# Performance work log

Hardware: AMD Instinct MI355X
Metric: run time of the kernel (lower is better)

Reference implementation:

```python
import jax, jax.numpy as jnp
import numpy as np

B, M, FIN, FOUT, K, E = 4, 50000, 128, 128, 4, 800000


def setup_inputs() -> dict:
    key = jax.random.key(0)
    ks = jax.random.split(key, 8)
    x = jax.random.normal(ks[0], (B, M, FIN), dtype=jnp.float32)
    L_rows = jax.random.randint(ks[1], (E,), 0, M, dtype=jnp.int32)
    L_cols = jax.random.randint(ks[2], (E,), 0, M, dtype=jnp.int32)
    # stands in for the rescaled (0.75 * (2L/lmax - I)) Laplacian values
    L_vals = jax.random.normal(ks[3], (E,), dtype=jnp.float32) * 0.05
    stddev = 1.0 / np.sqrt(FIN * (K + 0.5) / 2.0)
    kernel = jax.random.normal(ks[4], (K * FIN, FOUT), dtype=jnp.float32) * stddev
    W_down = jax.random.normal(ks[5], (FOUT, FOUT // 8), dtype=jnp.float32) * (1.0 / np.sqrt(FOUT))
    b_down = jnp.zeros((FOUT // 8,), dtype=jnp.float32)
    W_up = jax.random.normal(ks[6], (FOUT // 8, FOUT), dtype=jnp.float32) * (1.0 / np.sqrt(FOUT // 8))
    b_up = jnp.zeros((FOUT,), dtype=jnp.float32)
    return {"x": x, "L_vals": L_vals, "L_rows": L_rows, "L_cols": L_cols,
            "kernel": kernel, "W_down": W_down, "b_down": b_down,
            "W_up": W_up, "b_up": b_up}


def reference(x, L_vals, L_rows, L_cols, kernel, W_down, b_down, W_up, b_up):
    B_, M_, Fin = x.shape
    K_ = kernel.shape[0] // Fin

    def spmm(X):  # sparse L [M,M] @ dense X [M, D]
        return jax.ops.segment_sum(L_vals[:, None] * X[L_cols], L_rows, num_segments=M_)

    # Chebyshev recurrence, operating on [M, Fin*B] like the TF code
    x0 = x.transpose(1, 2, 0).reshape(M_, Fin * B_)
    stack = [x0]
    if K_ > 1:
        x1 = spmm(x0)
        stack.append(x1)
    for _ in range(2, K_):
        x2 = 2.0 * spmm(x1) - x0
        stack.append(x2)
        x0, x1 = x1, x2

    # [K,M,Fin*B] -> [K,M,Fin,B] -> [B,M,Fin,K] -> [B*M, Fin*K]
    xs = jnp.stack(stack, axis=0).reshape(K_, M_, Fin, B_)
    xs = xs.transpose(3, 1, 2, 0).reshape(B_ * M_, Fin * K_)
    y = (xs @ kernel).reshape(B_, M_, -1)
    y = jax.nn.relu(y)

    # SE block: avg-pool over nodes, down (swish), up (sigmoid), scale
    s = jnp.mean(y, axis=1, keepdims=True)          # [B, 1, Fout]
    d = jax.nn.swish(s @ W_down + b_down)           # [B, 1, Fout/8]
    u = jax.nn.sigmoid(d @ W_up + b_up)             # [B, 1, Fout]
    return y * u
```

## Files before the change

kernel.cpp:

```cpp
#include <hip/hip_runtime.h>
#include <hip/hip_bf16.h>

#define BB 4
#define MM 50000
#define FINF 128
#define FOUTF 128
#define KCH 4
#define EE 800000
#define NROWS (BB*MM)
#define XC 512
#define CD 512
#define SLABS 4
#define SC (XC/SLABS)
#define SCB 512
#define NSB ((MM + SCB - 1)/SCB)
#define GXB ((MM + 255)/256)

__device__ __forceinline__ float bf2f(unsigned short u){
    union{unsigned int i; float f;} v; v.i = ((unsigned int)u) << 16; return v.f;
}
__device__ __forceinline__ unsigned short f2bf(float f){
    union{float f; unsigned int i;} v; v.f = f;
    unsigned int r = v.i + 0x7FFF + ((v.i >> 16) & 1);
    return (unsigned short)(r >> 16);
}

typedef __bf16 bf16x8 __attribute__((ext_vector_type(8)));
typedef float  f32x4  __attribute__((ext_vector_type(4)));

__global__ __launch_bounds__(256) void k_init_x0(const float* __restrict__ x,
                                                 unsigned short* __restrict__ X0){
    int tid = blockIdx.x*256 + threadIdx.x;
    if (tid >= BB*MM*FINF/4) return;
    int f4 = tid & 31;
    int t  = tid >> 5;
    int m  = t % MM, b = t / MM;
    float4 v = ((const float4*)x)[tid];
    ushort4 o;
    o.x = f2bf(v.x); o.y = f2bf(v.y); o.z = f2bf(v.z); o.w = f2bf(v.w);
    *(ushort4*)(X0 + (size_t)m*XC + b*FINF + f4*4) = o;
}

__global__ __launch_bounds__(256) void k_prepw(const float* __restrict__ kern,
                                               unsigned short* __restrict__ Wt){
    int tid = blockIdx.x*256 + threadIdx.x;
    int c = tid & 511, n = tid >> 9;
    int kc = c >> 7, f = c & 127;
    int ns = n >> 4, l16 = n & 15;
    int ks = c >> 5, rem = c & 31, g = rem >> 3, j = rem & 7;
    int lane = g*16 + l16;
    Wt[((ns*16 + ks)*64 + lane)*8 + j] = f2bf(kern[(f*KCH + kc)*FOUTF + n]);
}

__global__ __launch_bounds__(256) void k_hist(const int* __restrict__ rows, int* __restrict__ counts){
    int e = blockIdx.x*256 + threadIdx.x;
    if (e < EE) atomicAdd(&counts[rows[e]], 1);
}

__global__ __launch_bounds__(256) void k_scanA(const int* __restrict__ counts, int* __restrict__ part){
    __shared__ int red[256];
    int b = blockIdx.x, t = threadIdx.x;
    int i = b*SCB + t;
    int s = 0;
    if (i < MM) s += counts[i];
    if (i + 256 < (b+1)*SCB && i + 256 < MM) s += counts[i+256];
    red[t] = s; __syncthreads();
    for (int d = 128; d > 0; d >>= 1){
        if (t < d) red[t] += red[t+d];
        __syncthreads();
    }
    if (t == 0) part[b] = red[0];
}

__global__ __launch_bounds__(128) void k_scanB(int* __restrict__ part){
    __shared__ int sh[128];
    int t = threadIdx.x;
    sh[t] = (t < NSB) ? part[t] : 0;
    __syncthreads();
    for (int d = 1; d < 128; d <<= 1){
        int v = (t >= d) ? sh[t-d] : 0;
        __syncthreads();
        sh[t] += v;
        __syncthreads();
    }
    if (t < NSB) part[t] = sh[t];
}

__global__ __launch_bounds__(256) void k_scanC(const int* __restrict__ counts, const int* __restrict__ part,
                                               int* __restrict__ offs, int* __restrict__ cursor){
    __shared__ int sh[256];
    int b = blockIdx.x, t = threadIdx.x;
    int base = (b == 0) ? 0 : part[b-1];
    int i0 = b*SCB + 2*t;
    int c0 = (i0     < MM) ? counts[i0]   : 0;
    int c1 = (i0 + 1 < MM) ? counts[i0+1] : 0;
    sh[t] = c0 + c1; __syncthreads();
    for (int d = 1; d < 256; d <<= 1){
        int v = (t >= d) ? sh[t-d] : 0;
        __syncthreads();
        sh[t] += v;
        __syncthreads();
    }
    int excl = base + sh[t] - (c0 + c1);
    if (i0 < MM){ offs[i0] = excl;      cursor[i0] = excl; }
    if (i0 + 1 < MM){ offs[i0+1] = excl + c0; cursor[i0+1] = excl + c0; }
    if (b == gridDim.x-1 && t == 255) offs[MM] = EE;
}

__global__ __launch_bounds__(256) void k_scatter(const int* __restrict__ rows, const int* __restrict__ cols,
                                                 const float* __restrict__ vals, int* __restrict__ cursor,
                                                 int2* __restrict__ edges){
    int e = blockIdx.x*256 + threadIdx.x;
    if (e >= EE) return;
    int r = rows[e];
    int pos = atomicAdd(&cursor[r], 1);
    edges[pos] = make_int2(cols[e], __float_as_int(vals[e]));
}

__global__ __launch_bounds__(256) void k_spmm_slab(const unsigned short* __restrict__ Xin,
                                                   const unsigned short* __restrict__ Xprev,
                                                   unsigned short* __restrict__ Xout,
                                                   const int* __restrict__ offs,
                                                   const int2* __restrict__ edges,
                                                   float alpha, int sub, int cbase){
    int m    = blockIdx.x*4 + (threadIdx.x >> 6);
    int lane = threadIdx.x & 63;
    size_t c0 = (size_t)cbase + lane*2;
    int start = offs[m], end = offs[m+1];
    float a0 = 0.f, a1 = 0.f;

    int nb = (end - start) & ~3;
    int burst_end = start + nb;
    int j = start;

    int2 ee[4];
    if (j < burst_end){
        #pragma unroll
        for (int q = 0; q < 4; ++q) ee[q] = edges[j+q];
    }
    while (j < burst_end){
        int2 e_[4];
        #pragma unroll
        for (int q = 0; q < 4; ++q) e_[q] = ee[q];
        j += 4;
        if (j < burst_end){
            #pragma unroll
            for (int q = 0; q < 4; ++q) ee[q] = edges[j+q];
        }
        ushort2 xv[4];
        #pragma unroll
        for (int q = 0; q < 4; ++q)
            xv[q] = *(const ushort2*)(Xin + (size_t)e_[q].x*XC + c0);
        #pragma unroll
        for (int q = 0; q < 4; ++q){
            float val = __int_as_float(e_[q].y);
            a0 += val*bf2f(xv[q].x); a1 += val*bf2f(xv[q].y);
        }
    }
    for (; j < end; ++j){
        int2 e = edges[j];
        float val = __int_as_float(e.y);
        ushort2 xv = *(const ushort2*)(Xin + (size_t)e.x*XC + c0);
        a0 += val*bf2f(xv.x); a1 += val*bf2f(xv.y);
    }

    a0 *= alpha; a1 *= alpha;
    if (sub){
        ushort2 pv = *(const ushort2*)(Xprev + (size_t)m*XC + c0);
        a0 -= bf2f(pv.x); a1 -= bf2f(pv.y);
    }
    ushort2 o; o.x = f2bf(a0); o.y = f2bf(a1);
    *(ushort2*)(Xout + (size_t)m*XC + c0) = o;
}

__global__ __launch_bounds__(256, 2) void k_gemm(const unsigned short* __restrict__ X0,
                                                 const unsigned short* __restrict__ X1,
                                                 const unsigned short* __restrict__ X2,
                                                 const unsigned short* __restrict__ X3,
                                                 const unsigned short* __restrict__ Wt,
                                                 float* __restrict__ Y,
                                                 float* __restrict__ Ypart){
    const int wave = threadIdx.x >> 6;
    const int lane = threadIdx.x & 63;
    const int l16  = lane & 15;
    const int g    = lane >> 4;
    const int bidx = blockIdx.y;
    const int m0   = blockIdx.x*256 + wave*64;

    int aoff[4];
    #pragma unroll
    for (int i = 0; i < 4; ++i){
        int mr = m0 + i*16 + l16;
        if (mr >= MM) mr = MM-1;
        aoff[i] = mr*XC + bidx*FINF + g*8;
    }

    const unsigned short* const Xs[4] = {X0, X1, X2, X3};

    f32x4 acc[4][8];
    #pragma unroll
    for (int i = 0; i < 4; ++i)
        #pragma unroll
        for (int j = 0; j < 8; ++j) acc[i][j] = (f32x4){0.f,0.f,0.f,0.f};

    bf16x8 a_cur[4], b_cur[8], a_nxt[4], b_nxt[8];

    {
        const unsigned short* Xb = Xs[0];
        #pragma unroll
        for (int i = 0; i < 4; ++i) a_cur[i] = *(const bf16x8*)(Xb + aoff[i]);
        #pragma unroll
        for (int ns = 0; ns < 8; ++ns) b_cur[ns] = *(const bf16x8*)(Wt + (ns*16)*512 + lane*8);
    }

    #pragma unroll
    for (int ks = 0; ks < 16; ++ks){
        if (ks < 15){
            const int kn = ks + 1;
            const unsigned short* Xb = Xs[kn >> 2];
            const int f0 = (kn & 3)*32;
            #pragma unroll
            for (int i = 0; i < 4; ++i) a_nxt[i] = *(const bf16x8*)(Xb + aoff[i] + f0);
            #pragma unroll
            for (int ns = 0; ns < 8; ++ns) b_nxt[ns] = *(const bf16x8*)(Wt + (ns*16 + kn)*512 + lane*8);
        }
        #pragma unroll
        for (int ns = 0; ns < 8; ++ns)
            #pragma unroll
            for (int i = 0; i < 4; ++i)
                acc[i][ns] = __builtin_amdgcn_mfma_f32_16x16x32_bf16(a_cur[i], b_cur[ns], acc[i][ns], 0, 0, 0);
        #pragma unroll
        for (int i = 0; i < 4; ++i) a_cur[i] = a_nxt[i];
        #pragma unroll
        for (int ns = 0; ns < 8; ++ns) b_cur[ns] = b_nxt[ns];
    }

    __shared__ float ldsum[4][FOUTF];
    float csum[8];
    #pragma unroll
    for (int ns = 0; ns < 8; ++ns) csum[ns] = 0.f;

    #pragma unroll
    for (int i = 0; i < 4; ++i){
        #pragma unroll
        for (int reg = 0; reg < 4; ++reg){
            int mr = m0 + i*16 + g*4 + reg;
            if (mr < MM){
                #pragma unroll
                for (int ns = 0; ns < 8; ++ns){
                    float v = acc[i][ns][reg];
                    v = v > 0.f ? v : 0.f;
                    Y[((size_t)bidx*MM + mr)*FOUTF + ns*16 + l16] = v;
                    csum[ns] += v;
                }
            }
        }
    }
    #pragma unroll
    for (int ns = 0; ns < 8; ++ns){
        float v = csum[ns];
        v += __shfl_xor(v, 16);
        v += __shfl_xor(v, 32);
        csum[ns] = v;
    }
    if (lane < 16){
        #pragma unroll
        for (int ns = 0; ns < 8; ++ns) ldsum[wave][ns*16 + lane] = csum[ns];
    }
    __syncthreads();
    int t = threadIdx.x;
    if (t < FOUTF){
        float s = ldsum[0][t] + ldsum[1][t] + ldsum[2][t] + ldsum[3][t];
        Ypart[((size_t)bidx*GXB + blockIdx.x)*FOUTF + t] = s;
    }
}

__global__ __launch_bounds__(128) void k_se(const float* __restrict__ Ypart,
                                            const float* __restrict__ Wd, const float* __restrict__ bd,
                                            const float* __restrict__ Wu, const float* __restrict__ bu,
                                            float* __restrict__ u){
    int b = blockIdx.x, t = threadIdx.x;
    __shared__ float sm[128];
    __shared__ float dsh[16];
    float s = 0.f;
    for (int j = 0; j < GXB; ++j) s += Ypart[((size_t)b*GXB + j)*FOUTF + t];
    sm[t] = s * (1.0f/MM);
    __syncthreads();
    if (t < 16){
        float a = bd[t];
        for (int f = 0; f < 128; ++f) a += sm[f]*Wd[f*16 + t];
        dsh[t] = a / (1.f + expf(-a));
    }
    __syncthreads();
    float a = bu[t];
    for (int j = 0; j < 16; ++j) a += dsh[j]*Wu[j*FOUTF + t];
    u[b*FOUTF + t] = 1.f/(1.f + expf(-a));
}

__global__ __launch_bounds__(256) void k_scale(const float* __restrict__ Y, const float* __restrict__ u,
                                               float* __restrict__ out){
    int tid = blockIdx.x*256 + threadIdx.x;
    if (tid >= NROWS*FOUTF/4) return;
    int b  = tid / (MM*FOUTF/4);
    int f4 = tid & 31;
    float4 yv = ((const float4*)Y)[tid];
    float4 uv = *(const float4*)(u + b*FOUTF + f4*4);
    float4 o;
    o.x = yv.x*uv.x; o.y = yv.y*uv.y; o.z = yv.z*uv.z; o.w = yv.w*uv.w;
    ((float4*)out)[tid] = o;
}

extern "C" void kernel_launch(void* const* d_in, const int* in_sizes, int n_in,
                              void* d_out, int out_size, void* d_ws, size_t ws_size,
                              hipStream_t stream){
    (void)in_sizes; (void)n_in; (void)out_size; (void)ws_size;
    const float* x    = (const float*)d_in[0];
    const float* lv   = (const float*)d_in[1];
    const int*   lr   = (const int*)d_in[2];
    const int*   lc   = (const int*)d_in[3];
    const float* kern = (const float*)d_in[4];
    const float* Wd   = (const float*)d_in[5];
    const float* bd   = (const float*)d_in[6];
    const float* Wu   = (const float*)d_in[7];
    const float* bu   = (const float*)d_in[8];
    float* out = (float*)d_out;

    char* w = (char*)d_ws;
    size_t off = 0;
    auto take = [&](size_t bytes)->char*{
        char* p = w + off; off += (bytes + 255) & ~(size_t)255; return p;
    };
    unsigned short* X[4];
    for (int i = 0; i < 4; ++i) X[i] = (unsigned short*)take((size_t)MM*XC*2);
    float* Y           = (float*)take((size_t)NROWS*FOUTF*4);
    unsigned short* Wt = (unsigned short*)take((size_t)FOUTF*CD*2);
    int* counts        = (int*)take((size_t)MM*4);
    int* offs          = (int*)take((size_t)(MM+1)*4);
    int* cursor        = (int*)take((size_t)MM*4);
    int2* edges        = (int2*)take((size_t)EE*8);
    int* part          = (int*)take((size_t)NSB*4);
    float* Ypart       = (float*)take((size_t)BB*GXB*FOUTF*4);
    float* u           = (float*)take((size_t)BB*FOUTF*4);

    hipMemsetAsync(counts, 0, MM*4, stream);

    k_init_x0<<<25000, 256, 0, stream>>>(x, X[0]);
    k_prepw<<<256, 256, 0, stream>>>(kern, Wt);
    k_hist<<<(EE+255)/256, 256, 0, stream>>>(lr, counts);
    k_scanA<<<NSB, 256, 0, stream>>>(counts, part);
    k_scanB<<<1, 128, 0, stream>>>(part);
    k_scanC<<<NSB, 256, 0, stream>>>(counts, part, offs, cursor);
    k_scatter<<<(EE+255)/256, 256, 0, stream>>>(lr, lc, lv, cursor, edges);

    for (int s = 0; s < SLABS; ++s){
        int cbase = s*SC;
        k_spmm_slab<<<MM/4, 256, 0, stream>>>(X[0], X[0], X[1], offs, edges, 1.0f, 0, cbase);
        k_spmm_slab<<<MM/4, 256, 0, stream>>>(X[1], X[0], X[2], offs, edges, 2.0f, 1, cbase);
        k_spmm_slab<<<MM/4, 256, 0, stream>>>(X[2], X[1], X[3], offs, edges, 2.0f, 1, cbase);
    }

    dim3 ggemm(GXB, BB);
    k_gemm<<<ggemm, 256, 0, stream>>>(X[0], X[1], X[2], X[3], Wt, Y, Ypart);

    k_se<<<BB, 128, 0, stream>>>(Ypart, Wd, bd, Wu, bu, u);
    k_scale<<<25000, 256, 0, stream>>>(Y, u, out);
}
```

Before: 833.0 us.

## Stage GEMM A/B tiles through swizzled double-buffered LDS via direct global-to-LDS loads

The dense Chebyshev GEMM now copies the A (node features) and B (weights) tiles into two LDS buffers with `global_load_lds`, instead of each wave loading its operands straight into registers. The A tile uses an XOR swizzle so the later LDS reads avoid bank conflicts. Each weight tile is now loaded once per block and shared across all four waves, where before every wave fetched it separately. The cost is two barriers per k-step, more LDS use that may reduce occupancy, and reliance on the barrier to wait for the async LDS writes.

```diff
diff --git a/kernel.cpp b/kernel.cpp
--- a/kernel.cpp
+++ b/kernel.cpp
@@ -28,6 +28,9 @@
 typedef __bf16 bf16x8 __attribute__((ext_vector_type(8)));
 typedef float  f32x4  __attribute__((ext_vector_type(4)));
 
+typedef __attribute__((address_space(3))) unsigned int       lds_uint;
+typedef const __attribute__((address_space(1))) unsigned int gbl_uint;
+
 __global__ __launch_bounds__(256) void k_init_x0(const float* __restrict__ x,
                                                  unsigned short* __restrict__ X0){
     int tid = blockIdx.x*256 + threadIdx.x;
@@ -185,15 +188,10 @@
     const int l16  = lane & 15;
     const int g    = lane >> 4;
     const int bidx = blockIdx.y;
-    const int m0   = blockIdx.x*256 + wave*64;
-
-    int aoff[4];
-    #pragma unroll
-    for (int i = 0; i < 4; ++i){
-        int mr = m0 + i*16 + l16;
-        if (mr >= MM) mr = MM-1;
-        aoff[i] = mr*XC + bidx*FINF + g*8;
-    }
+    const int m0   = blockIdx.x*256;
+
+    __shared__ unsigned short As[2][8192];
+    __shared__ unsigned short Bs[2][4096];
 
     const unsigned short* const Xs[4] = {X0, X1, X2, X3};
 
@@ -203,36 +201,49 @@
         #pragma unroll
         for (int j = 0; j < 8; ++j) acc[i][j] = (f32x4){0.f,0.f,0.f,0.f};
 
-    bf16x8 a_cur[4], b_cur[8], a_nxt[4], b_nxt[8];
-
-    {
-        const unsigned short* Xb = Xs[0];
-        #pragma unroll
-        for (int i = 0; i < 4; ++i) a_cur[i] = *(const bf16x8*)(Xb + aoff[i]);
-        #pragma unroll
-        for (int ns = 0; ns < 8; ++ns) b_cur[ns] = *(const bf16x8*)(Wt + (ns*16)*512 + lane*8);
-    }
-
-    #pragma unroll
+    auto stage = [&](int buf, int ks){
+        const unsigned short* Xb = Xs[ks >> 2];
+        const int f0 = (ks & 3)*64;
+        #pragma unroll
+        for (int q = 0; q < 4; ++q){
+            int row = q*64 + wave*16 + (lane >> 2);
+            int mr  = m0 + row; if (mr >= MM) mr = MM-1;
+            int inner = ((lane & 3)*16) ^ ((row & 6) << 3);
+            const char* src = (const char*)Xb + (size_t)mr*1024 + bidx*256 + f0 + inner;
+            lds_uint* dst = (lds_uint*)(&As[buf][(q*4096 + wave*1024)/2]);
+            __builtin_amdgcn_global_load_lds((gbl_uint*)src, dst, 16, 0, 0);
+        }
+        #pragma unroll
+        for (int q = 0; q < 2; ++q){
+            int ns = q*4 + wave;
+            const char* src = (const char*)Wt + (size_t)(ns*16 + ks)*1024 + lane*16;
+            lds_uint* dst = (lds_uint*)(&Bs[buf][ns*512]);
+            __builtin_amdgcn_global_load_lds((gbl_uint*)src, dst, 16, 0, 0);
+        }
+    };
+
+    stage(0, 0);
+    __syncthreads();
+
     for (int ks = 0; ks < 16; ++ks){
-        if (ks < 15){
-            const int kn = ks + 1;
-            const unsigned short* Xb = Xs[kn >> 2];
-            const int f0 = (kn & 3)*32;
-            #pragma unroll
-            for (int i = 0; i < 4; ++i) a_nxt[i] = *(const bf16x8*)(Xb + aoff[i] + f0);
-            #pragma unroll
-            for (int ns = 0; ns < 8; ++ns) b_nxt[ns] = *(const bf16x8*)(Wt + (ns*16 + kn)*512 + lane*8);
-        }
-        #pragma unroll
-        for (int ns = 0; ns < 8; ++ns)
+        const int buf = ks & 1;
+        if (ks < 15) stage(buf ^ 1, ks + 1);
+
+        bf16x8 a[4];
+        #pragma unroll
+        for (int i = 0; i < 4; ++i){
+            int rr = wave*64 + i*16 + l16;
+            int phys = rr*64 + ((g*16) ^ ((rr & 6) << 3));
+            a[i] = *(const bf16x8*)((const char*)&As[buf][0] + phys);
+        }
+        #pragma unroll
+        for (int ns = 0; ns < 8; ++ns){
+            bf16x8 b = *(const bf16x8*)(&Bs[buf][ns*512 + lane*8]);
             #pragma unroll
             for (int i = 0; i < 4; ++i)
-                acc[i][ns] = __builtin_amdgcn_mfma_f32_16x16x32_bf16(a_cur[i], b_cur[ns], acc[i][ns], 0, 0, 0);
-        #pragma unroll
-        for (int i = 0; i < 4; ++i) a_cur[i] = a_nxt[i];
-        #pragma unroll
-        for (int ns = 0; ns < 8; ++ns) b_cur[ns] = b_nxt[ns];
+                acc[i][ns] = __builtin_amdgcn_mfma_f32_16x16x32_bf16(a[i], b, acc[i][ns], 0, 0, 0);
+        }
+        __syncthreads();
     }
 
     __shared__ float ldsum[4][FOUTF];
@@ -244,7 +255,7 @@
     for (int i = 0; i < 4; ++i){
         #pragma unroll
         for (int reg = 0; reg < 4; ++reg){
-            int mr = m0 + i*16 + g*4 + reg;
+            int mr = m0 + wave*64 + i*16 + g*4 + reg;
             if (mr < MM){
                 #pragma unroll
                 for (int ns = 0; ns < 8; ++ns){
```

After: 790.9 us. -5.1%, faster.
